# Performance work log

Measured on AMD Instinct MI355X. Metric: run time of the kernel, lower is better.

The kernel has to match this reference:

```python
import jax, jax.numpy as jnp
import numpy as np

B, L, HID = 8, 1025, 1024
H, KV, DH = 16, 4, 64
EPS = 1e-6
ROPE_BASE = 10000.0


def _rms_norm(x, w):
    var = jnp.mean(jnp.square(x), axis=-1, keepdims=True)
    return x * jax.lax.rsqrt(var + EPS) * w


def _rotate_half(x):
    x1, x2 = jnp.split(x, 2, axis=-1)
    return jnp.concatenate([-x2, x1], axis=-1)


def _rope_cache(seq_len, dim):
    inv_freq = 1.0 / (ROPE_BASE ** (jnp.arange(0, dim, 2, dtype=jnp.float32) / dim))
    pos = jnp.arange(seq_len, dtype=jnp.float32)
    freqs = pos[:, None] * inv_freq[None, :]            # [L_img, dim/2]
    emb = jnp.concatenate([freqs, freqs], axis=-1)       # [L_img, dim]
    return jnp.cos(emb), jnp.sin(emb)


def setup_inputs() -> dict:
    key = jax.random.key(0)
    ks = jax.random.split(key, 5)
    s_in = 1.0
    s_q = float(np.sqrt(2.0 / (HID + H * DH)))
    s_kv = float(np.sqrt(2.0 / (HID + KV * DH)))
    s_o = float(np.sqrt(2.0 / (H * DH + HID)) / np.sqrt(2.0))
    return {
        "inputs": jax.random.normal(ks[0], (B, L, HID), jnp.float32) * s_in,
        "Wq": jax.random.normal(ks[1], (H * DH, HID), jnp.float32) * s_q,
        "Wk": jax.random.normal(ks[2], (KV * DH, HID), jnp.float32) * s_kv,
        "Wv": jax.random.normal(ks[3], (KV * DH, HID), jnp.float32) * s_kv,
        "Wo": jax.random.normal(ks[4], (HID, H * DH), jnp.float32) * s_o,
        "q_norm_w": jnp.ones((DH,), jnp.float32),
        "k_norm_w": jnp.ones((DH,), jnp.float32),
    }


def reference(inputs, Wq, Wk, Wv, Wo, q_norm_w, k_norm_w):
    b, l, _ = inputs.shape
    # projections (torch Linear: x @ W.T), reshape to heads, QK RMSNorm
    q = (inputs @ Wq.T).reshape(b, l, H, DH)
    k = (inputs @ Wk.T).reshape(b, l, KV, DH)
    v = (inputs @ Wv.T).reshape(b, l, KV, DH)
    q = _rms_norm(q, q_norm_w).transpose(0, 2, 1, 3)    # [B,H,L,DH]
    k = _rms_norm(k, k_norm_w).transpose(0, 2, 1, 3)    # [B,KV,L,DH]
    v = v.transpose(0, 2, 1, 3)                          # [B,KV,L,DH]

    # RoPE only on image tokens (skip first action token)
    l_img = l - 1
    cos, sin = _rope_cache(l_img, DH)                    # [L_img, DH]
    cos = cos[None, None].astype(q.dtype)
    sin = sin[None, None].astype(q.dtype)
    q_img = q[:, :, 1:]
    k_img = k[:, :, 1:]
    q = jnp.concatenate([q[:, :, :1], q_img * cos + _rotate_half(q_img) * sin], axis=2)
    k = jnp.concatenate([k[:, :, :1], k_img * cos + _rotate_half(k_img) * sin], axis=2)

    # GQA: repeat kv heads
    rep = H // KV
    k = jnp.repeat(k, rep, axis=1)                       # [B,H,L,DH]
    v = jnp.repeat(v, rep, axis=1)

    # manual attention: NOTE no 1/sqrt(DH) scaling (faithful to source)
    scores = jnp.einsum("bhqd,bhkd->bhqk", q, k)
    attn = jax.nn.softmax(scores.astype(jnp.float32), axis=-1).astype(q.dtype)
    out = jnp.einsum("bhqk,bhkd->bhqd", attn, v)         # [B,H,L,DH]
    out = out.transpose(0, 2, 1, 3).reshape(b, l, H * DH)
    return out @ Wo.T
```

## Files before the change

kernel.cpp:

```cpp
#include <hip/hip_runtime.h>
#include <hip/hip_bf16.h>

using bf16 = __hip_bfloat16;
typedef __bf16 bf16x8 __attribute__((ext_vector_type(8)));
typedef float f32x4 __attribute__((ext_vector_type(4)));
typedef short short8 __attribute__((ext_vector_type(8)));
typedef unsigned short ushort4v __attribute__((ext_vector_type(4)));

#define MFMA16(a, b, c) __builtin_amdgcn_mfma_f32_16x16x32_bf16((a), (b), (c), 0, 0, 0)

constexpr int B_ = 8, L_ = 1025, H_ = 16, KV_ = 4;
constexpr int LKP_ = 1088;
constexpr int M_ = B_ * L_;

constexpr int NX = 8396800, NWQ = 1048576, NWK = 262144, NWV = 262144,
              NWO = 1048576, NNW = 64;

template <int NWG>
__device__ __forceinline__ int xcd_swz(int orig) {
  constexpr int q = NWG >> 3, r = NWG & 7;
  const int x = orig & 7, idx = orig >> 3;
  return (x < r ? x * (q + 1) : r * (q + 1) + (x - r) * q) + idx;
}

__global__ __launch_bounds__(64) void detect_dtype(const unsigned short* qw_raw,
                                                   int* flag) {
  if (threadIdx.x == 0) flag[0] = (qw_raw[0] == 0x3F80) ? 0 : 1;
}

__global__ __launch_bounds__(256) void convert_all(
    const void* s0, const void* s1, const void* s2, const void* s3,
    const void* s4, const void* s5, const void* s6,
    bf16* d0, bf16* d1, bf16* d2, bf16* d3, bf16* d4, bf16* d5, bf16* d6,
    const int* flag) {
  const int f = *flag;
  const int tid = blockIdx.x * blockDim.x + threadIdx.x;
  const int stride = gridDim.x * blockDim.x;
  auto conv = [&](const void* s, bf16* d, int n) {
    const int n8 = n >> 3;
    if (f) {
      const f32x4* sf = (const f32x4*)s;
      short8* dd = (short8*)d;
      for (int i = tid; i < n8; i += stride) {
        const f32x4 v0 = sf[2 * i], v1 = sf[2 * i + 1];
        short8 o;
#pragma unroll
        for (int j = 0; j < 4; ++j) {
          o[j]     = __builtin_bit_cast(short, __float2bfloat16(v0[j]));
          o[j + 4] = __builtin_bit_cast(short, __float2bfloat16(v1[j]));
        }
        dd[i] = o;
      }
    } else {
      const short8* su = (const short8*)s;
      short8* dd = (short8*)d;
      for (int i = tid; i < n8; i += stride) dd[i] = su[i];
    }
  };
  conv(s0, d0, NX);
  conv(s1, d1, NWQ);
  conv(s2, d2, NWK);
  conv(s3, d3, NWV);
  conv(s4, d4, NWO);
  conv(s5, d5, NNW);
  conv(s6, d6, NNW);
}

__global__ __launch_bounds__(256) void zero_pads(bf16* Kb, bf16* VT) {
  const int idx = blockIdx.x * 256 + threadIdx.x;
  const bf16 z = __float2bfloat16(0.f);
  {
    const int g = idx / 4032, rem = idx % 4032;
    const int r = rem >> 6, d = rem & 63;
    Kb[((size_t)g * LKP_ + 1025 + r) * 64 + d] = z;
  }
  {
    const int row = idx / 63, c = idx % 63;
    VT[(size_t)row * LKP_ + 1025 + c] = z;
  }
}

template <int EPI, int NT, int NWG>
__global__ __launch_bounds__(512) void gemm_bt(
    const bf16* __restrict__ X, const bf16* __restrict__ W0,
    const bf16* __restrict__ W1, const bf16* __restrict__ W2,
    void* __restrict__ O0, bf16* __restrict__ O1, bf16* __restrict__ O2,
    const bf16* __restrict__ qw, const bf16* __restrict__ kw,
    const int* flag) {
  const int wg = xcd_swz<NWG>(blockIdx.x);
  const int m0 = (wg / NT) * 128;
  const int n0 = (wg % NT) * 128;

  int outf32 = 0;
  if constexpr (EPI == 0) outf32 = *flag;

  const bf16* W;
  int nw0;
  if constexpr (EPI == 0) {
    W = W0; nw0 = n0;
  } else {
    if (n0 < 1024)      { W = W0; nw0 = n0; }
    else if (n0 < 1280) { W = W1; nw0 = n0 - 1024; }
    else                { W = W2; nw0 = n0 - 1280; }
  }

  __shared__ bf16 As[2][128 * 32];
  __shared__ bf16 Bs[2][128 * 32];

  const int tid = threadIdx.x;
  const int lane = tid & 63, wid = tid >> 6;
  const int wr = wid >> 1, wc = wid & 1;
  const int lo = lane & 15, g = lane >> 4;

  const f32x4 zero4 = {0.f, 0.f, 0.f, 0.f};
  f32x4 acc[2][4];
#pragma unroll
  for (int i = 0; i < 2; ++i)
#pragma unroll
    for (int j = 0; j < 4; ++j) acc[i][j] = zero4;

  const int rr = tid >> 2, cb = tid & 3;
  const int wofs = rr * 32 + ((cb ^ ((rr >> 1) & 3)) * 8);
  int xr = m0 + rr; if (xr > M_ - 1) xr = M_ - 1;
  const bf16* xp = X + (size_t)xr * 1024 + cb * 8;
  const bf16* wp = W + (size_t)(nw0 + rr) * 1024 + cb * 8;

  short8 ra = *reinterpret_cast<const short8*>(xp); xp += 32;
  short8 rb = *reinterpret_cast<const short8*>(wp); wp += 32;

  const int swl = (g ^ ((lo >> 1) & 3)) * 8;

  for (int kt = 0; kt < 32; ++kt) {
    const int cur = kt & 1;
    __syncthreads();
    *reinterpret_cast<short8*>(&As[cur][wofs]) = ra;
    *reinterpret_cast<short8*>(&Bs[cur][wofs]) = rb;
    __syncthreads();

    if (kt < 31) {
      ra = *reinterpret_cast<const short8*>(xp); xp += 32;
      rb = *reinterpret_cast<const short8*>(wp); wp += 32;
    }

    bf16x8 a[2], bb[4];
#pragma unroll
    for (int i = 0; i < 2; ++i)
      a[i] = *reinterpret_cast<const bf16x8*>(&As[cur][(wr * 32 + i * 16 + lo) * 32 + swl]);
#pragma unroll
    for (int j = 0; j < 4; ++j)
      bb[j] = *reinterpret_cast<const bf16x8*>(&Bs[cur][(wc * 64 + j * 16 + lo) * 32 + swl]);
#pragma unroll
    for (int i = 0; i < 2; ++i)
#pragma unroll
      for (int j = 0; j < 4; ++j)
        acc[i][j] = MFMA16(a[i], bb[j], acc[i][j]);
  }

  const bool qkreg = (EPI == 1) && (n0 < 1280);
  float wv[4];
  float invf0 = 0.f, invf1 = 0.f;
  if (qkreg) {
    const bf16* w = (n0 < 1024) ? qw : kw;
#pragma unroll
    for (int j = 0; j < 4; ++j) wv[j] = __bfloat162float(w[j * 16 + lo]);
    constexpr float c = -0.41524101186092029f;
    invf0 = exp2f((float)lo * c);
    invf1 = invf0 * exp2f(16.f * c);
  }

#pragma unroll
  for (int i = 0; i < 2; ++i) {
#pragma unroll
    for (int ii = 0; ii < 4; ++ii) {
      const int m = m0 + wr * 32 + i * 16 + g * 4 + ii;
      if (m >= M_) continue;
      const int b = m / L_;
      const int l = m % L_;
      float fv[4];
#pragma unroll
      for (int j = 0; j < 4; ++j) fv[j] = acc[i][j][ii];

      if (qkreg) {
#pragma unroll
        for (int j = 0; j < 4; ++j)
          fv[j] = __bfloat162float(__float2bfloat16(fv[j]));
        float ss = fv[0] * fv[0] + fv[1] * fv[1] + fv[2] * fv[2] + fv[3] * fv[3];
        ss += __shfl_xor(ss, 1);
        ss += __shfl_xor(ss, 2);
        ss += __shfl_xor(ss, 4);
        ss += __shfl_xor(ss, 8);
        const float r = rsqrtf(ss * (1.f / 64.f) + 1e-6f);
#pragma unroll
        for (int j = 0; j < 4; ++j) fv[j] *= r * wv[j];
        if (l > 0) {
          const float pos = (float)(l - 1);
          float sn0, cs0, sn1, cs1;
          __sincosf(pos * invf0, &sn0, &cs0);
          __sincosf(pos * invf1, &sn1, &cs1);
          const float a0 = fv[0], a2 = fv[2];
          fv[0] = a0 * cs0 - a2 * sn0;
          fv[2] = a2 * cs0 + a0 * sn0;
          const float a1 = fv[1], a3 = fv[3];
          fv[1] = a1 * cs1 - a3 * sn1;
          fv[3] = a3 * cs1 + a1 * sn1;
        }
      }

#pragma unroll
      for (int j = 0; j < 4; ++j) {
        const int n = n0 + wc * 64 + j * 16 + lo;
        const float f = fv[j];
        if constexpr (EPI == 0) {
          if (outf32) ((float*)O0)[(size_t)m * 1024 + n] = f;
          else        ((bf16*)O0)[(size_t)m * 1024 + n] = __float2bfloat16(f);
        } else {
          const bf16 v = __float2bfloat16(f);
          if (n < 1024) {
            ((bf16*)O0)[((size_t)(b * H_ + (n >> 6)) * L_ + l) * 64 + (n & 63)] = v;
          } else if (n < 1280) {
            const int c2 = n - 1024;
            O1[((size_t)(b * KV_ + (c2 >> 6)) * LKP_ + l) * 64 + (c2 & 63)] = v;
          } else {
            const int c2 = n - 1280;
            O2[((size_t)(b * KV_ + (c2 >> 6)) * 64 + (c2 & 63)) * LKP_ + l] = v;
          }
        }
      }
    }
  }
}

__global__ __launch_bounds__(512) void attn(
    const bf16* __restrict__ Q, const bf16* __restrict__ Kt,
    const bf16* __restrict__ VT, bf16* __restrict__ AO) {
  const int tid = threadIdx.x, lane = tid & 63, w = tid >> 6;
  const int lo = lane & 15, g = lane >> 4;
  const int qt = blockIdx.x, h = blockIdx.y, b = blockIdx.z;
  const int kv = h >> 2;

  __shared__ unsigned short Ks[64 * 64];
  __shared__ unsigned short Vs[64 * 64];
  __shared__ unsigned short Ps[8 * 16 * 64];

  const bf16* qbase = Q + (size_t)(b * H_ + h) * L_ * 64;
  int qrow = qt * 128 + w * 16 + lo;
  if (qrow > L_ - 1) qrow = L_ - 1;
  const bf16x8 qf0 = *reinterpret_cast<const bf16x8*>(qbase + (size_t)qrow * 64 + g * 8);
  const bf16x8 qf1 = *reinterpret_cast<const bf16x8*>(qbase + (size_t)qrow * 64 + 32 + g * 8);

  const f32x4 zero4 = {0.f, 0.f, 0.f, 0.f};
  f32x4 o[4];
  float mi = -3e38f, li = 0.f;
#pragma unroll
  for (int i = 0; i < 4; ++i) o[i] = zero4;

  const int sr = tid >> 3;
  const int scol = (tid & 7) * 8;
  const int swcol = ((tid & 7) ^ (sr & 7)) * 8;
  const bf16* kptr = Kt + ((size_t)(b * KV_ + kv) * LKP_ + sr) * 64 + scol;
  const bf16* vptr = VT + ((size_t)(b * KV_ + kv) * 64 + sr) * LKP_ + scol;

  const int sw0 = (g ^ (lo & 7)) * 8;
  const int sw1 = ((4 | g) ^ (lo & 7)) * 8;

  short8 ka = *reinterpret_cast<const short8*>(kptr);
  short8 va = *reinterpret_cast<const short8*>(vptr);

  for (int kt = 0; kt < 17; ++kt) {
    __syncthreads();
    *reinterpret_cast<short8*>(&Ks[sr * 64 + swcol]) = ka;
    *reinterpret_cast<short8*>(&Vs[sr * 64 + swcol]) = va;
    __syncthreads();

    if (kt < 16) {
      kptr += 64 * 64;
      vptr += 64;
      ka = *reinterpret_cast<const short8*>(kptr);
      va = *reinterpret_cast<const short8*>(vptr);
    }

    f32x4 s[4];
    __builtin_amdgcn_s_setprio(1);
#pragma unroll
    for (int kb = 0; kb < 4; ++kb) {
      f32x4 t = zero4;
      const bf16x8 ka0 = *reinterpret_cast<const bf16x8*>(&Ks[(kb * 16 + lo) * 64 + sw0]);
      const bf16x8 ka1 = *reinterpret_cast<const bf16x8*>(&Ks[(kb * 16 + lo) * 64 + sw1]);
      t = MFMA16(ka0, qf0, t);
      t = MFMA16(ka1, qf1, t);
      s[kb] = t;
    }
    __builtin_amdgcn_s_setprio(0);
    if (kt == 16) {
#pragma unroll
      for (int kb = 0; kb < 4; ++kb)
#pragma unroll
        for (int i = 0; i < 4; ++i)
          if (kt * 64 + kb * 16 + g * 4 + i >= L_) s[kb][i] = -1e30f;
    }

    float t0 = fmaxf(fmaxf(s[0][0], s[0][1]), fmaxf(s[0][2], s[0][3]));
    float t1 = fmaxf(fmaxf(s[1][0], s[1][1]), fmaxf(s[1][2], s[1][3]));
    float t2 = fmaxf(fmaxf(s[2][0], s[2][1]), fmaxf(s[2][2], s[2][3]));
    float t3 = fmaxf(fmaxf(s[3][0], s[3][1]), fmaxf(s[3][2], s[3][3]));
    float tm = fmaxf(fmaxf(t0, t1), fmaxf(t2, t3));
    tm = fmaxf(tm, __shfl_xor(tm, 16));
    tm = fmaxf(tm, __shfl_xor(tm, 32));
    if (!__all(tm <= mi)) {
      const float mn = fmaxf(mi, tm);
      const float sc = __expf(mi - mn);
      mi = mn;
      li *= sc;
#pragma unroll
      for (int db = 0; db < 4; ++db)
#pragma unroll
        for (int i = 0; i < 4; ++i) o[db][i] *= sc;
    }
#pragma unroll
    for (int kb = 0; kb < 4; ++kb)
#pragma unroll
      for (int i = 0; i < 4; ++i) s[kb][i] = __expf(s[kb][i] - mi);
    float p0 = (s[0][0] + s[0][1]) + (s[0][2] + s[0][3]);
    float p1 = (s[1][0] + s[1][1]) + (s[1][2] + s[1][3]);
    float p2 = (s[2][0] + s[2][1]) + (s[2][2] + s[2][3]);
    float p3 = (s[3][0] + s[3][1]) + (s[3][2] + s[3][3]);
    float ps = (p0 + p1) + (p2 + p3);
    ps += __shfl_xor(ps, 16);
    ps += __shfl_xor(ps, 32);
    li += ps;

#pragma unroll
    for (int kb = 0; kb < 4; ++kb) {
      ushort4v pk;
#pragma unroll
      for (int i = 0; i < 4; ++i)
        pk[i] = __builtin_bit_cast(unsigned short, __float2bfloat16(s[kb][i]));
      const int pblk = (2 * kb + (g >> 1)) ^ (lo & 7);
      *reinterpret_cast<ushort4v*>(&Ps[w * 1024 + lo * 64 + pblk * 8 + (g & 1) * 4]) = pk;
    }

    const bf16x8 pb0 = *reinterpret_cast<const bf16x8*>(&Ps[w * 1024 + lo * 64 + sw0]);
    const bf16x8 pb1 = *reinterpret_cast<const bf16x8*>(&Ps[w * 1024 + lo * 64 + sw1]);
    __builtin_amdgcn_s_setprio(1);
#pragma unroll
    for (int db = 0; db < 4; ++db) {
      const bf16x8 va0 = *reinterpret_cast<const bf16x8*>(&Vs[(db * 16 + lo) * 64 + sw0]);
      const bf16x8 va1 = *reinterpret_cast<const bf16x8*>(&Vs[(db * 16 + lo) * 64 + sw1]);
      o[db] = MFMA16(va0, pb0, o[db]);
      o[db] = MFMA16(va1, pb1, o[db]);
    }
    __builtin_amdgcn_s_setprio(0);
  }

  const int qr = qt * 128 + w * 16 + lo;
  if (qr < L_) {
    const float inv = 1.f / li;
    unsigned* base = (unsigned*)(AO + ((size_t)b * L_ + qr) * 1024 + h * 64);
#pragma unroll
    for (int db = 0; db < 4; ++db) {
#pragma unroll
      for (int i2 = 0; i2 < 4; i2 += 2) {
        const unsigned u0 = __builtin_bit_cast(unsigned short,
                                __float2bfloat16(o[db][i2] * inv));
        const unsigned u1 = __builtin_bit_cast(unsigned short,
                                __float2bfloat16(o[db][i2 + 1] * inv));
        base[(db * 16 + 4 * g + i2) >> 1] = u0 | (u1 << 16);
      }
    }
  }
}

extern "C" void kernel_launch(void* const* d_in, const int* in_sizes, int n_in,
                              void* d_out, int out_size, void* d_ws, size_t ws_size,
                              hipStream_t stream) {
  (void)in_sizes; (void)n_in; (void)out_size; (void)ws_size;

  char* wsb = (char*)d_ws;
  int* flagp = (int*)wsb;
  bf16* cX  = (bf16*)(wsb + 16);
  bf16* cWq = cX + NX;
  bf16* cWk = cWq + NWQ;
  bf16* cWv = cWk + NWK;
  bf16* cWo = cWv + NWV;
  bf16* cqw = cWo + NWO;
  bf16* ckw = cqw + NNW;
  bf16* Qb  = ckw + NNW;
  bf16* Kb  = Qb  + (size_t)B_ * H_ * L_ * 64;
  bf16* VTb = Kb  + (size_t)B_ * KV_ * LKP_ * 64;
  bf16* AOb = VTb + (size_t)B_ * KV_ * 64 * LKP_;

  detect_dtype<<<1, 64, 0, stream>>>((const unsigned short*)d_in[5], flagp);
  convert_all<<<2048, 256, 0, stream>>>(
      d_in[0], d_in[1], d_in[2], d_in[3], d_in[4], d_in[5], d_in[6],
      cX, cWq, cWk, cWv, cWo, cqw, ckw, flagp);
  zero_pads<<<504, 256, 0, stream>>>(Kb, VTb);

  gemm_bt<1, 12, 780><<<780, 512, 0, stream>>>(cX, cWq, cWk, cWv, Qb, Kb, VTb,
                                               cqw, ckw, nullptr);
  attn<<<dim3(9, 16, 8), 512, 0, stream>>>(Qb, Kb, VTb, AOb);
  gemm_bt<0, 8, 520><<<520, 512, 0, stream>>>(AOb, cWo, nullptr, nullptr, d_out,
                                              nullptr, nullptr, nullptr, nullptr,
                                              flagp);
}
```

Measured before the change: 214.5 us.

## Fuse fp32-to-bf16 input conversion into GEMM tile loads

Removes the separate convert_all pass that copied inputs and weights to bf16 workspace buffers. The GEMMs now read the raw inputs directly and convert fp32 to bf16 in registers before the LDS store, and the norm weights are read according to the runtime dtype flag. This saves a full read-and-write pass over about 8M activations plus the weights and one launch. In exchange the GEMM global loads double in width when inputs are fp32, and the weight tiles get reconverted by every workgroup that reads them.

```diff
diff --git a/kernel.cpp b/kernel.cpp
--- a/kernel.cpp
+++ b/kernel.cpp
@@ -13,9 +13,6 @@
 constexpr int LKP_ = 1088;
 constexpr int M_ = B_ * L_;
 
-constexpr int NX = 8396800, NWQ = 1048576, NWK = 262144, NWV = 262144,
-              NWO = 1048576, NNW = 64;
-
 template <int NWG>
 __device__ __forceinline__ int xcd_swz(int orig) {
   constexpr int q = NWG >> 3, r = NWG & 7;
@@ -26,44 +23,6 @@
 __global__ __launch_bounds__(64) void detect_dtype(const unsigned short* qw_raw,
                                                    int* flag) {
   if (threadIdx.x == 0) flag[0] = (qw_raw[0] == 0x3F80) ? 0 : 1;
-}
-
-__global__ __launch_bounds__(256) void convert_all(
-    const void* s0, const void* s1, const void* s2, const void* s3,
-    const void* s4, const void* s5, const void* s6,
-    bf16* d0, bf16* d1, bf16* d2, bf16* d3, bf16* d4, bf16* d5, bf16* d6,
-    const int* flag) {
-  const int f = *flag;
-  const int tid = blockIdx.x * blockDim.x + threadIdx.x;
-  const int stride = gridDim.x * blockDim.x;
-  auto conv = [&](const void* s, bf16* d, int n) {
-    const int n8 = n >> 3;
-    if (f) {
-      const f32x4* sf = (const f32x4*)s;
-      short8* dd = (short8*)d;
-      for (int i = tid; i < n8; i += stride) {
-        const f32x4 v0 = sf[2 * i], v1 = sf[2 * i + 1];
-        short8 o;
-#pragma unroll
-        for (int j = 0; j < 4; ++j) {
-          o[j]     = __builtin_bit_cast(short, __float2bfloat16(v0[j]));
-          o[j + 4] = __builtin_bit_cast(short, __float2bfloat16(v1[j]));
-        }
-        dd[i] = o;
-      }
-    } else {
-      const short8* su = (const short8*)s;
-      short8* dd = (short8*)d;
-      for (int i = tid; i < n8; i += stride) dd[i] = su[i];
-    }
-  };
-  conv(s0, d0, NX);
-  conv(s1, d1, NWQ);
-  conv(s2, d2, NWK);
-  conv(s3, d3, NWV);
-  conv(s4, d4, NWO);
-  conv(s5, d5, NNW);
-  conv(s6, d6, NNW);
 }
 
 __global__ __launch_bounds__(256) void zero_pads(bf16* Kb, bf16* VT) {
@@ -82,27 +41,28 @@
 
 template <int EPI, int NT, int NWG>
 __global__ __launch_bounds__(512) void gemm_bt(
-    const bf16* __restrict__ X, const bf16* __restrict__ W0,
-    const bf16* __restrict__ W1, const bf16* __restrict__ W2,
+    const void* __restrict__ Xv, const void* __restrict__ W0v,
+    const void* __restrict__ W1v, const void* __restrict__ W2v,
     void* __restrict__ O0, bf16* __restrict__ O1, bf16* __restrict__ O2,
-    const bf16* __restrict__ qw, const bf16* __restrict__ kw,
-    const int* flag) {
+    const void* __restrict__ qwv, const void* __restrict__ kwv,
+    const int* __restrict__ flag) {
+  const int f32in = *flag;
   const int wg = xcd_swz<NWG>(blockIdx.x);
   const int m0 = (wg / NT) * 128;
   const int n0 = (wg % NT) * 128;
 
-  int outf32 = 0;
-  if constexpr (EPI == 0) outf32 = *flag;
-
-  const bf16* W;
+  const void* Wv;
   int nw0;
   if constexpr (EPI == 0) {
-    W = W0; nw0 = n0;
+    Wv = W0v; nw0 = n0;
   } else {
-    if (n0 < 1024)      { W = W0; nw0 = n0; }
-    else if (n0 < 1280) { W = W1; nw0 = n0 - 1024; }
-    else                { W = W2; nw0 = n0 - 1280; }
-  }
+    if (n0 < 1024)      { Wv = W0v; nw0 = n0; }
+    else if (n0 < 1280) { Wv = W1v; nw0 = n0 - 1024; }
+    else                { Wv = W2v; nw0 = n0 - 1280; }
+  }
+
+  const bool af32 = (EPI == 1) && (f32in != 0);
+  const bool bf32 = (f32in != 0);
 
   __shared__ bf16 As[2][128 * 32];
   __shared__ bf16 Bs[2][128 * 32];
@@ -122,24 +82,60 @@
   const int rr = tid >> 2, cb = tid & 3;
   const int wofs = rr * 32 + ((cb ^ ((rr >> 1) & 3)) * 8);
   int xr = m0 + rr; if (xr > M_ - 1) xr = M_ - 1;
-  const bf16* xp = X + (size_t)xr * 1024 + cb * 8;
-  const bf16* wp = W + (size_t)(nw0 + rr) * 1024 + cb * 8;
-
-  short8 ra = *reinterpret_cast<const short8*>(xp); xp += 32;
-  short8 rb = *reinterpret_cast<const short8*>(wp); wp += 32;
+  const char* xp = (const char*)Xv + ((size_t)xr * 1024 + cb * 8) * (af32 ? 4 : 2);
+  const char* wp = (const char*)Wv + ((size_t)(nw0 + rr) * 1024 + cb * 8) * (bf32 ? 4 : 2);
+  const int xstep = af32 ? 128 : 64;
+  const int wstep = bf32 ? 128 : 64;
+
+  f32x4 ra0, ra1, rb0, rb1;
+  auto loadA = [&] {
+    ra0 = *(const f32x4*)xp;
+    if (af32) ra1 = *(const f32x4*)(xp + 16);
+    xp += xstep;
+  };
+  auto loadB = [&] {
+    rb0 = *(const f32x4*)wp;
+    if (bf32) rb1 = *(const f32x4*)(wp + 16);
+    wp += wstep;
+  };
+  auto packA = [&]() -> short8 {
+    if (af32) {
+      short8 o;
+#pragma unroll
+      for (int j = 0; j < 4; ++j) {
+        o[j]     = __builtin_bit_cast(short, __float2bfloat16(ra0[j]));
+        o[j + 4] = __builtin_bit_cast(short, __float2bfloat16(ra1[j]));
+      }
+      return o;
+    }
+    return __builtin_bit_cast(short8, ra0);
+  };
+  auto packB = [&]() -> short8 {
+    if (bf32) {
+      short8 o;
+#pragma unroll
+      for (int j = 0; j < 4; ++j) {
+        o[j]     = __builtin_bit_cast(short, __float2bfloat16(rb0[j]));
+        o[j + 4] = __builtin_bit_cast(short, __float2bfloat16(rb1[j]));
+      }
+      return o;
+    }
+    return __builtin_bit_cast(short8, rb0);
+  };
+
+  loadA(); loadB();
 
   const int swl = (g ^ ((lo >> 1) & 3)) * 8;
 
   for (int kt = 0; kt < 32; ++kt) {
     const int cur = kt & 1;
     __syncthreads();
-    *reinterpret_cast<short8*>(&As[cur][wofs]) = ra;
-    *reinterpret_cast<short8*>(&Bs[cur][wofs]) = rb;
+    *reinterpret_cast<short8*>(&As[cur][wofs]) = packA();
+    *reinterpret_cast<short8*>(&Bs[cur][wofs]) = packB();
     __syncthreads();
 
     if (kt < 31) {
-      ra = *reinterpret_cast<const short8*>(xp); xp += 32;
-      rb = *reinterpret_cast<const short8*>(wp); wp += 32;
+      loadA(); loadB();
     }
 
     bf16x8 a[2], bb[4];
@@ -160,9 +156,13 @@
   float wv[4];
   float invf0 = 0.f, invf1 = 0.f;
   if (qkreg) {
-    const bf16* w = (n0 < 1024) ? qw : kw;
-#pragma unroll
-    for (int j = 0; j < 4; ++j) wv[j] = __bfloat162float(w[j * 16 + lo]);
+    const void* w = (n0 < 1024) ? qwv : kwv;
+#pragma unroll
+    for (int j = 0; j < 4; ++j) {
+      float wf = f32in ? ((const float*)w)[j * 16 + lo]
+                       : __bfloat162float(((const bf16*)w)[j * 16 + lo]);
+      wv[j] = __bfloat162float(__float2bfloat16(wf));
+    }
     constexpr float c = -0.41524101186092029f;
     invf0 = exp2f((float)lo * c);
     invf1 = invf0 * exp2f(16.f * c);
@@ -211,8 +211,8 @@
         const int n = n0 + wc * 64 + j * 16 + lo;
         const float f = fv[j];
         if constexpr (EPI == 0) {
-          if (outf32) ((float*)O0)[(size_t)m * 1024 + n] = f;
-          else        ((bf16*)O0)[(size_t)m * 1024 + n] = __float2bfloat16(f);
+          if (f32in) ((float*)O0)[(size_t)m * 1024 + n] = f;
+          else       ((bf16*)O0)[(size_t)m * 1024 + n] = __float2bfloat16(f);
         } else {
           const bf16 v = __float2bfloat16(f);
           if (n < 1024) {
@@ -377,28 +377,18 @@
 
   char* wsb = (char*)d_ws;
   int* flagp = (int*)wsb;
-  bf16* cX  = (bf16*)(wsb + 16);
-  bf16* cWq = cX + NX;
-  bf16* cWk = cWq + NWQ;
-  bf16* cWv = cWk + NWK;
-  bf16* cWo = cWv + NWV;
-  bf16* cqw = cWo + NWO;
-  bf16* ckw = cqw + NNW;
-  bf16* Qb  = ckw + NNW;
+  bf16* Qb  = (bf16*)(wsb + 16);
   bf16* Kb  = Qb  + (size_t)B_ * H_ * L_ * 64;
   bf16* VTb = Kb  + (size_t)B_ * KV_ * LKP_ * 64;
   bf16* AOb = VTb + (size_t)B_ * KV_ * 64 * LKP_;
 
   detect_dtype<<<1, 64, 0, stream>>>((const unsigned short*)d_in[5], flagp);
-  convert_all<<<2048, 256, 0, stream>>>(
-      d_in[0], d_in[1], d_in[2], d_in[3], d_in[4], d_in[5], d_in[6],
-      cX, cWq, cWk, cWv, cWo, cqw, ckw, flagp);
   zero_pads<<<504, 256, 0, stream>>>(Kb, VTb);
 
-  gemm_bt<1, 12, 780><<<780, 512, 0, stream>>>(cX, cWq, cWk, cWv, Qb, Kb, VTb,
-                                               cqw, ckw, nullptr);
+  gemm_bt<1, 12, 780><<<780, 512, 0, stream>>>(
+      d_in[0], d_in[1], d_in[2], d_in[3], Qb, Kb, VTb, d_in[5], d_in[6], flagp);
   attn<<<dim3(9, 16, 8), 512, 0, stream>>>(Qb, Kb, VTb, AOb);
-  gemm_bt<0, 8, 520><<<520, 512, 0, stream>>>(AOb, cWo, nullptr, nullptr, d_out,
-                                              nullptr, nullptr, nullptr, nullptr,
-                                              flagp);
-}
+  gemm_bt<0, 8, 520><<<520, 512, 0, stream>>>(
+      AOb, d_in[4], nullptr, nullptr, d_out, nullptr, nullptr, nullptr, nullptr,
+      flagp);
+}
```

Result: no change. 217.7 us (+1.5%).
